# Kernel optimization log

Measured on AMD Instinct MI355X. Metric: run time of the kernel, lower is better.

Reference implementation:

```python
import jax, jax.numpy as jnp
import numpy as np

B, C, D_MODEL, N_HEADS = 2, 2048, 1024, 16


def rotary_matrix(context_length: int, d: int) -> jnp.ndarray:
    """Faithful vectorization of get_rotary_matrix: theta = 10000^(-2*(i-1)/d)."""
    half = d // 2
    i = jnp.arange(half, dtype=jnp.float32)
    theta = 10000.0 ** (-2.0 * (i - 1.0) / d)          # note the (i-1), as in source
    m = jnp.arange(context_length, dtype=jnp.float32)
    ang = m[:, None] * theta                            # [C, d/2]
    c, s = jnp.cos(ang), jnp.sin(ang)
    ev = 2 * jnp.arange(half)
    od = ev + 1
    R = jnp.zeros((context_length, d, d), jnp.float32)
    R = R.at[:, ev, ev].set(c)
    R = R.at[:, ev, od].set(-s)
    R = R.at[:, od, ev].set(s)
    R = R.at[:, od, od].set(c)
    return R


def setup_inputs() -> dict:
    key = jax.random.key(0)
    k1, k2, k3, k4 = jax.random.split(key, 4)
    x = jax.random.normal(k1, (B, C, D_MODEL), dtype=jnp.float32)
    w_qkv = jax.random.normal(k2, (3 * D_MODEL, D_MODEL), dtype=jnp.float32) * 0.02
    w_out = jax.random.normal(k3, (D_MODEL, D_MODEL), dtype=jnp.float32) * 0.02
    b_out = jax.random.normal(k4, (D_MODEL,), dtype=jnp.float32) * 0.02
    return {"x": x, "w_qkv": w_qkv, "w_out": w_out, "b_out": b_out}


def reference(x, w_qkv, w_out, b_out):
    b, c, d = x.shape
    h = N_HEADS
    dh = d // h
    qkv = x @ w_qkv.T                                   # [B,C,3D]
    q, k, v = jnp.split(qkv, 3, axis=-1)
    # [B,C,D] -> [B,H,C,dh]
    q = q.reshape(b, c, h, dh).transpose(0, 2, 1, 3)
    k = k.reshape(b, c, h, dh).transpose(0, 2, 1, 3)
    v = v.reshape(b, c, h, dh).transpose(0, 2, 1, 3)
    R = rotary_matrix(c, dh)                            # [C,dh,dh]
    q_rot = jnp.einsum('bhci,cij->bhcj', q, R)
    k_rot = jnp.einsum('bhci,cij->bhcj', k, R)
    scale = jnp.sqrt(jnp.float32(dh))
    # exact math of the source: exp with no max subtraction, separate num/den
    attn_num = jnp.exp(jnp.einsum('bhqd,bhkd->bhqk', q_rot, k_rot) / scale)
    attn_den = jnp.exp(jnp.einsum('bhqd,bhkd->bhqk', q, k) / scale)
    attn_den = jnp.sum(attn_den, axis=-1, keepdims=True)
    attn = attn_num / attn_den
    causal = jnp.tril(jnp.ones((c, c), jnp.float32))[None, None]
    attn = jnp.where(causal == 0, 0.0, attn)
    y = jnp.einsum('bhqk,bhkd->bhqd', attn, v)
    y = y.transpose(0, 2, 1, 3).reshape(b, c, d)
    return y @ w_out.T + b_out
```

## Files before the change

kernel.cpp:

```cpp
#include <hip/hip_runtime.h>
#include <math.h>
#include <stdint.h>

#define BB 2
#define CC 2048
#define DD 1024
#define HH 16
#define DHH 64
#define HALF 32

typedef __attribute__((ext_vector_type(8))) short bf16x8;
typedef __attribute__((ext_vector_type(4))) float f32x4;
typedef unsigned int u32;

__device__ __forceinline__ ushort f2bf(float f) {
    uint32_t u = __builtin_bit_cast(uint32_t, f);
    u = (u + 0x7FFFu + ((u >> 16) & 1u)) >> 16;
    return (ushort)u;
}
__device__ __forceinline__ float bf2f(ushort u) {
    return __builtin_bit_cast(float, ((uint32_t)u) << 16);
}

__device__ __forceinline__ void gload16(const void* g, void* lds) {
    __builtin_amdgcn_global_load_lds(
        (const u32 __attribute__((address_space(1)))*)g,
        (u32 __attribute__((address_space(3)))*)lds, 16, 0, 0);
}

__global__ __launch_bounds__(256) void cast_bf16_k(const float* __restrict__ src,
                                                   ushort* __restrict__ dst, int n8) {
    int id = blockIdx.x * 256 + threadIdx.x;
    if (id >= n8) return;
    float4 a = *reinterpret_cast<const float4*>(src + (size_t)id * 8);
    float4 b = *reinterpret_cast<const float4*>(src + (size_t)id * 8 + 4);
    bf16x8 o;
    o[0] = (short)f2bf(a.x); o[1] = (short)f2bf(a.y);
    o[2] = (short)f2bf(a.z); o[3] = (short)f2bf(a.w);
    o[4] = (short)f2bf(b.x); o[5] = (short)f2bf(b.y);
    o[6] = (short)f2bf(b.z); o[7] = (short)f2bf(b.w);
    *reinterpret_cast<bf16x8*>(dst + (size_t)id * 8) = o;
}

__global__ __launch_bounds__(256) void rope_table_k(float* __restrict__ ct, float* __restrict__ st) {
    int idx = blockIdx.x * 256 + threadIdx.x;
    if (idx >= CC * HALF) return;
    int m = idx >> 5;
    int t = idx & 31;
    double theta_d = pow(10000.0, -2.0 * ((double)t - 1.0) / 64.0);
    float theta = (float)theta_d;
    float ang = (float)m * theta;
    ct[idx] = cosf(ang);
    st[idx] = sinf(ang);
}

__global__ __launch_bounds__(256) void qkv_gemm_mfma_k(const ushort* __restrict__ xb,
                                                       const ushort* __restrict__ wqb,
                                                       ushort* __restrict__ q,
                                                       ushort* __restrict__ k,
                                                       ushort* __restrict__ vT) {
    __shared__ ushort Al[128 * 64];
    __shared__ ushort Bl[128 * 64];
    const int tid = threadIdx.x;
    const int w = tid >> 6, l = tid & 63;
    const int l15 = l & 15, lg = l >> 4;
    const int wr = w >> 1, wc = w & 1;
    const int m0 = blockIdx.x * 128, n0 = blockIdx.y * 128;
    const int lrow = l >> 3, lch = l & 7;

    f32x4 acc[4][4];
#pragma unroll
    for (int i = 0; i < 4; i++)
#pragma unroll
        for (int j = 0; j < 4; j++) acc[i][j] = (f32x4){0.f, 0.f, 0.f, 0.f};

    for (int k0 = 0; k0 < 1024; k0 += 64) {
        __syncthreads();
#pragma unroll
        for (int c = 0; c < 4; c++) {
            int row = w * 32 + c * 8 + lrow;
            int gch = (lch ^ (row & 7)) * 8;
            gload16(xb + (size_t)(m0 + row) * 1024 + k0 + gch, &Al[(w * 32 + c * 8) * 64]);
            gload16(wqb + (size_t)(n0 + row) * 1024 + k0 + gch, &Bl[(w * 32 + c * 8) * 64]);
        }
        __syncthreads();
#pragma unroll
        for (int kk = 0; kk < 2; kk++) {
            bf16x8 a[4], b[4];
#pragma unroll
            for (int mt = 0; mt < 4; mt++) {
                int row = wr * 64 + mt * 16 + l15;
                a[mt] = *reinterpret_cast<const bf16x8*>(&Al[row * 64 + ((kk * 4 + lg) ^ (row & 7)) * 8]);
            }
#pragma unroll
            for (int nt = 0; nt < 4; nt++) {
                int row = wc * 64 + nt * 16 + l15;
                b[nt] = *reinterpret_cast<const bf16x8*>(&Bl[row * 64 + ((kk * 4 + lg) ^ (row & 7)) * 8]);
            }
#pragma unroll
            for (int mt = 0; mt < 4; mt++)
#pragma unroll
                for (int nt = 0; nt < 4; nt++)
                    acc[mt][nt] = __builtin_amdgcn_mfma_f32_16x16x32_bf16(a[mt], b[nt], acc[mt][nt], 0, 0, 0);
        }
    }
#pragma unroll
    for (int mt = 0; mt < 4; mt++)
#pragma unroll
        for (int nt = 0; nt < 4; nt++) {
            int n = n0 + wc * 64 + nt * 16 + l15;
            int part = n >> 10;
            int d = n & 1023;
            int h = d >> 6, dd = d & 63;
            int mbase = m0 + wr * 64 + mt * 16 + lg * 4;
            int bb = mbase >> 11, cpos = mbase & 2047;
            if (part == 2) {
                ushort4 pk;
                pk.x = f2bf(acc[mt][nt][0]); pk.y = f2bf(acc[mt][nt][1]);
                pk.z = f2bf(acc[mt][nt][2]); pk.w = f2bf(acc[mt][nt][3]);
                *reinterpret_cast<ushort4*>(vT + (((size_t)bb * HH + h) * DHH + dd) * CC + cpos) = pk;
            } else {
                ushort* dst = (part == 0) ? q : k;
#pragma unroll
                for (int r = 0; r < 4; r++)
                    dst[(((size_t)bb * HH + h) * CC + (cpos + r)) * DHH + dd] = f2bf(acc[mt][nt][r]);
            }
        }
}

__global__ __launch_bounds__(256) void rot_k(const ushort* __restrict__ q, const ushort* __restrict__ k,
                                             const float* __restrict__ ct, const float* __restrict__ st,
                                             ushort* __restrict__ qr, ushort* __restrict__ kr) {
    int id = blockIdx.x * 256 + threadIdx.x;
    int oct = id & 7;
    int c = (id >> 3) & 2047;
    int bh = id >> 14;
    size_t base = ((size_t)bh * CC + c) * DHH + oct * 8;
    bf16x8 q8 = *reinterpret_cast<const bf16x8*>(q + base);
    bf16x8 k8 = *reinterpret_cast<const bf16x8*>(k + base);
    float4 c4 = *reinterpret_cast<const float4*>(ct + c * 32 + oct * 4);
    float4 s4 = *reinterpret_cast<const float4*>(st + c * 32 + oct * 4);
    float cc[4] = {c4.x, c4.y, c4.z, c4.w};
    float ss[4] = {s4.x, s4.y, s4.z, s4.w};
    bf16x8 qo, ko;
#pragma unroll
    for (int p = 0; p < 4; p++) {
        float qe = bf2f((ushort)q8[2 * p]), qd = bf2f((ushort)q8[2 * p + 1]);
        float ke = bf2f((ushort)k8[2 * p]), kd = bf2f((ushort)k8[2 * p + 1]);
        qo[2 * p]     = (short)f2bf(qe * cc[p] + qd * ss[p]);
        qo[2 * p + 1] = (short)f2bf(qd * cc[p] - qe * ss[p]);
        ko[2 * p]     = (short)f2bf(ke * cc[p] + kd * ss[p]);
        ko[2 * p + 1] = (short)f2bf(kd * cc[p] - ke * ss[p]);
    }
    *reinterpret_cast<bf16x8*>(qr + base) = qo;
    *reinterpret_cast<bf16x8*>(kr + base) = ko;
}

#define PSTR 76
__global__ __launch_bounds__(256) void attn_mfma_k(const ushort* __restrict__ qg,
                                                   const ushort* __restrict__ kg,
                                                   const ushort* __restrict__ vTg,
                                                   const ushort* __restrict__ qrg,
                                                   const ushort* __restrict__ krg,
                                                   ushort* __restrict__ y) {
    __shared__ ushort Kl[64 * 64];
    __shared__ ushort Krl[64 * 64];
    __shared__ ushort Vt[64 * 64];
    __shared__ ushort Pl[4][16 * PSTR];

    const int tid = threadIdx.x;
    const int w = tid >> 6, l = tid & 63;
    const int l15 = l & 15, lg = l >> 4;
    const int lrow = l >> 3, lch = l & 7;
    const int bid = blockIdx.x;
    const int bh = bid >> 5;
    const int xt = bid & 31;
    const int tile = (bid & 512) ? (31 - xt) : xt;
    const int q0 = tile * 64;
    const ushort* qb  = qg  + (size_t)bh * CC * DHH;
    const ushort* kb  = kg  + (size_t)bh * CC * DHH;
    const ushort* vTb = vTg + (size_t)bh * DHH * CC;
    const ushort* qrb = qrg + (size_t)bh * CC * DHH;
    const ushort* krb = krg + (size_t)bh * CC * DHH;

    bf16x8 qf[2], qrf[2];
#pragma unroll
    for (int kk = 0; kk < 2; kk++) {
        int row = q0 + w * 16 + l15;
        qf[kk]  = *reinterpret_cast<const bf16x8*>(qb  + (size_t)row * DHH + kk * 32 + lg * 8);
        qrf[kk] = *reinterpret_cast<const bf16x8*>(qrb + (size_t)row * DHH + kk * 32 + lg * 8);
    }

    f32x4 yacc[4];
    float dacc[4];
#pragma unroll
    for (int nt = 0; nt < 4; nt++) yacc[nt] = (f32x4){0.f, 0.f, 0.f, 0.f};
#pragma unroll
    for (int r = 0; r < 4; r++) dacc[r] = 0.f;

    for (int kt = 0; kt < CC / 64; kt++) {
        const int k0 = kt * 64;
        const bool need = (k0 <= q0 + 63);
        __syncthreads();
#pragma unroll
        for (int c = 0; c < 2; c++) {
            int row = w * 16 + c * 8 + lrow;
            int gch = (lch ^ (row & 7)) * 8;
            gload16(kb + (size_t)(k0 + row) * DHH + gch, &Kl[(w * 16 + c * 8) * 64]);
            if (need) {
                gload16(krb + (size_t)(k0 + row) * DHH + gch, &Krl[(w * 16 + c * 8) * 64]);
                gload16(vTb + (size_t)row * CC + k0 + gch, &Vt[(w * 16 + c * 8) * 64]);
            }
        }
        __syncthreads();

#pragma unroll
        for (int nt = 0; nt < 4; nt++) {
            f32x4 s = (f32x4){0.f, 0.f, 0.f, 0.f};
#pragma unroll
            for (int kk = 0; kk < 2; kk++) {
                int row = nt * 16 + l15;
                bf16x8 bk = *reinterpret_cast<const bf16x8*>(&Kl[row * 64 + ((kk * 4 + lg) ^ (row & 7)) * 8]);
                s = __builtin_amdgcn_mfma_f32_16x16x32_bf16(qf[kk], bk, s, 0, 0, 0);
            }
#pragma unroll
            for (int r = 0; r < 4; r++) dacc[r] += exp2f(s[r] * 0.1803368801f);
        }

        if (need) {
#pragma unroll
            for (int nt = 0; nt < 4; nt++) {
                f32x4 s = (f32x4){0.f, 0.f, 0.f, 0.f};
#pragma unroll
                for (int kk = 0; kk < 2; kk++) {
                    int row = nt * 16 + l15;
                    bf16x8 bk = *reinterpret_cast<const bf16x8*>(&Krl[row * 64 + ((kk * 4 + lg) ^ (row & 7)) * 8]);
                    s = __builtin_amdgcn_mfma_f32_16x16x32_bf16(qrf[kk], bk, s, 0, 0, 0);
                }
#pragma unroll
                for (int r = 0; r < 4; r++) {
                    int qrow = q0 + w * 16 + lg * 4 + r;
                    int key = k0 + nt * 16 + l15;
                    float p = (key <= qrow) ? exp2f(s[r] * 0.1803368801f) : 0.f;
                    Pl[w][(lg * 4 + r) * PSTR + nt * 16 + l15] = f2bf(p);
                }
            }
            bf16x8 pa[2];
#pragma unroll
            for (int kk2 = 0; kk2 < 2; kk2++)
                pa[kk2] = *reinterpret_cast<const bf16x8*>(&Pl[w][l15 * PSTR + kk2 * 32 + lg * 8]);
#pragma unroll
            for (int nt2 = 0; nt2 < 4; nt2++)
#pragma unroll
                for (int kk2 = 0; kk2 < 2; kk2++) {
                    int row = nt2 * 16 + l15;
                    bf16x8 bv = *reinterpret_cast<const bf16x8*>(&Vt[row * 64 + ((kk2 * 4 + lg) ^ (row & 7)) * 8]);
                    yacc[nt2] = __builtin_amdgcn_mfma_f32_16x16x32_bf16(pa[kk2], bv, yacc[nt2], 0, 0, 0);
                }
        }
    }

#pragma unroll
    for (int r = 0; r < 4; r++) {
        float vsum = dacc[r];
#pragma unroll
        for (int msk = 1; msk < 16; msk <<= 1) vsum += __shfl_xor(vsum, msk, 64);
        dacc[r] = vsum;
    }

    const int b = bh >> 4, h = bh & 15;
#pragma unroll
    for (int r = 0; r < 4; r++) {
        int row = q0 + w * 16 + lg * 4 + r;
        float inv = 1.f / dacc[r];
#pragma unroll
        for (int nt2 = 0; nt2 < 4; nt2++) {
            int d = nt2 * 16 + l15;
            y[((size_t)b * CC + row) * DD + h * DHH + d] = f2bf(yacc[nt2][r] * inv);
        }
    }
}

__global__ __launch_bounds__(256) void out_proj_mfma_k(const ushort* __restrict__ yb,
                                                       const ushort* __restrict__ wob,
                                                       const float* __restrict__ bias,
                                                       float* __restrict__ out) {
    __shared__ ushort Al[128 * 64];
    __shared__ ushort Bl[128 * 64];
    const int tid = threadIdx.x;
    const int w = tid >> 6, l = tid & 63;
    const int l15 = l & 15, lg = l >> 4;
    const int wr = w >> 1, wc = w & 1;
    const int m0 = blockIdx.x * 128, n0 = blockIdx.y * 128;
    const int lrow = l >> 3, lch = l & 7;

    f32x4 acc[4][4];
#pragma unroll
    for (int i = 0; i < 4; i++)
#pragma unroll
        for (int j = 0; j < 4; j++) acc[i][j] = (f32x4){0.f, 0.f, 0.f, 0.f};

    for (int k0 = 0; k0 < 1024; k0 += 64) {
        __syncthreads();
#pragma unroll
        for (int c = 0; c < 4; c++) {
            int row = w * 32 + c * 8 + lrow;
            int gch = (lch ^ (row & 7)) * 8;
            gload16(yb + (size_t)(m0 + row) * 1024 + k0 + gch, &Al[(w * 32 + c * 8) * 64]);
            gload16(wob + (size_t)(n0 + row) * 1024 + k0 + gch, &Bl[(w * 32 + c * 8) * 64]);
        }
        __syncthreads();
#pragma unroll
        for (int kk = 0; kk < 2; kk++) {
            bf16x8 a[4], b[4];
#pragma unroll
            for (int mt = 0; mt < 4; mt++) {
                int row = wr * 64 + mt * 16 + l15;
                a[mt] = *reinterpret_cast<const bf16x8*>(&Al[row * 64 + ((kk * 4 + lg) ^ (row & 7)) * 8]);
            }
#pragma unroll
            for (int nt = 0; nt < 4; nt++) {
                int row = wc * 64 + nt * 16 + l15;
                b[nt] = *reinterpret_cast<const bf16x8*>(&Bl[row * 64 + ((kk * 4 + lg) ^ (row & 7)) * 8]);
            }
#pragma unroll
            for (int mt = 0; mt < 4; mt++)
#pragma unroll
                for (int nt = 0; nt < 4; nt++)
                    acc[mt][nt] = __builtin_amdgcn_mfma_f32_16x16x32_bf16(a[mt], b[nt], acc[mt][nt], 0, 0, 0);
        }
    }
#pragma unroll
    for (int mt = 0; mt < 4; mt++)
#pragma unroll
        for (int nt = 0; nt < 4; nt++) {
            int n = n0 + wc * 64 + nt * 16 + l15;
            float bv = bias[n];
#pragma unroll
            for (int r = 0; r < 4; r++) {
                int m = m0 + wr * 64 + mt * 16 + lg * 4 + r;
                out[(size_t)m * 1024 + n] = acc[mt][nt][r] + bv;
            }
        }
}

extern "C" void kernel_launch(void* const* d_in, const int* in_sizes, int n_in,
                              void* d_out, int out_size, void* d_ws, size_t ws_size,
                              hipStream_t stream) {
    (void)in_sizes; (void)n_in; (void)out_size; (void)ws_size;
    const float* x     = (const float*)d_in[0];
    const float* w_qkv = (const float*)d_in[1];
    const float* w_out = (const float*)d_in[2];
    const float* b_out = (const float*)d_in[3];
    float* out = (float*)d_out;

    char* p = (char*)d_ws;
    float* ct = (float*)p;  p += (size_t)CC * HALF * 4;
    float* st = (float*)p;  p += (size_t)CC * HALF * 4;
    ushort* xb  = (ushort*)p; p += (size_t)4096 * 1024 * 2;
    ushort* wqb = (ushort*)p; p += (size_t)3072 * 1024 * 2;
    ushort* wob = (ushort*)p; p += (size_t)1024 * 1024 * 2;
    const size_t TEN = (size_t)BB * HH * CC * DHH;
    ushort* qb = (ushort*)p; p += TEN * 2;
    ushort* kb = (ushort*)p; p += TEN * 2;
    ushort* vT = (ushort*)p; p += TEN * 2;
    ushort* qr = (ushort*)p; p += TEN * 2;
    ushort* kr = (ushort*)p; p += TEN * 2;
    ushort* yb = (ushort*)p; p += (size_t)4096 * 1024 * 2;

    cast_bf16_k<<<dim3(2048), dim3(256), 0, stream>>>(x, xb, 524288);
    cast_bf16_k<<<dim3(1536), dim3(256), 0, stream>>>(w_qkv, wqb, 393216);
    cast_bf16_k<<<dim3(512),  dim3(256), 0, stream>>>(w_out, wob, 131072);
    rope_table_k<<<dim3((CC * HALF) / 256), dim3(256), 0, stream>>>(ct, st);
    qkv_gemm_mfma_k<<<dim3(32, 24), dim3(256), 0, stream>>>(xb, wqb, qb, kb, vT);
    rot_k<<<dim3(2048), dim3(256), 0, stream>>>(qb, kb, ct, st, qr, kr);
    attn_mfma_k<<<dim3(1024), dim3(256), 0, stream>>>(qb, kb, vT, qr, kr, yb);
    out_proj_mfma_k<<<dim3(32, 8), dim3(256), 0, stream>>>(yb, wob, b_out, out);
}
```

Before: 179.6 us.

## Fuse RoPE into QKV GEMM epilogue and double-buffer attention K/V tiles

The separate rotary kernel is removed. The rotation is now applied in the QKV GEMM epilogue, using a lane shuffle to fetch the even/odd partner, and q/k plus qr/kr are written directly. The attention kernel double-buffers its K, Kr and V LDS tiles so the next tile loads while the current one computes, and it swaps the MFMA operand order so the score tile is transposed. That transposition lets the denominator reduction drop to two shuffles and lets P be written as packed 8-byte stores. The cost is doubled LDS use, which may lower occupancy, plus extra scattered table reads in the GEMM epilogue.

```diff
diff --git a/kernel.cpp b/kernel.cpp
--- a/kernel.cpp
+++ b/kernel.cpp
@@ -56,8 +56,12 @@
 
 __global__ __launch_bounds__(256) void qkv_gemm_mfma_k(const ushort* __restrict__ xb,
                                                        const ushort* __restrict__ wqb,
+                                                       const float* __restrict__ ct,
+                                                       const float* __restrict__ st,
                                                        ushort* __restrict__ q,
                                                        ushort* __restrict__ k,
+                                                       ushort* __restrict__ qr,
+                                                       ushort* __restrict__ kr,
                                                        ushort* __restrict__ vT) {
     __shared__ ushort Al[128 * 64];
     __shared__ ushort Bl[128 * 64];
@@ -120,52 +124,35 @@
                 pk.z = f2bf(acc[mt][nt][2]); pk.w = f2bf(acc[mt][nt][3]);
                 *reinterpret_cast<ushort4*>(vT + (((size_t)bb * HH + h) * DHH + dd) * CC + cpos) = pk;
             } else {
-                ushort* dst = (part == 0) ? q : k;
-#pragma unroll
-                for (int r = 0; r < 4; r++)
-                    dst[(((size_t)bb * HH + h) * CC + (cpos + r)) * DHH + dd] = f2bf(acc[mt][nt][r]);
-            }
-        }
-}
-
-__global__ __launch_bounds__(256) void rot_k(const ushort* __restrict__ q, const ushort* __restrict__ k,
-                                             const float* __restrict__ ct, const float* __restrict__ st,
-                                             ushort* __restrict__ qr, ushort* __restrict__ kr) {
-    int id = blockIdx.x * 256 + threadIdx.x;
-    int oct = id & 7;
-    int c = (id >> 3) & 2047;
-    int bh = id >> 14;
-    size_t base = ((size_t)bh * CC + c) * DHH + oct * 8;
-    bf16x8 q8 = *reinterpret_cast<const bf16x8*>(q + base);
-    bf16x8 k8 = *reinterpret_cast<const bf16x8*>(k + base);
-    float4 c4 = *reinterpret_cast<const float4*>(ct + c * 32 + oct * 4);
-    float4 s4 = *reinterpret_cast<const float4*>(st + c * 32 + oct * 4);
-    float cc[4] = {c4.x, c4.y, c4.z, c4.w};
-    float ss[4] = {s4.x, s4.y, s4.z, s4.w};
-    bf16x8 qo, ko;
-#pragma unroll
-    for (int p = 0; p < 4; p++) {
-        float qe = bf2f((ushort)q8[2 * p]), qd = bf2f((ushort)q8[2 * p + 1]);
-        float ke = bf2f((ushort)k8[2 * p]), kd = bf2f((ushort)k8[2 * p + 1]);
-        qo[2 * p]     = (short)f2bf(qe * cc[p] + qd * ss[p]);
-        qo[2 * p + 1] = (short)f2bf(qd * cc[p] - qe * ss[p]);
-        ko[2 * p]     = (short)f2bf(ke * cc[p] + kd * ss[p]);
-        ko[2 * p + 1] = (short)f2bf(kd * cc[p] - ke * ss[p]);
-    }
-    *reinterpret_cast<bf16x8*>(qr + base) = qo;
-    *reinterpret_cast<bf16x8*>(kr + base) = ko;
-}
-
-#define PSTR 76
+                ushort* dstu = (part == 0) ? q : k;
+                ushort* dstr = (part == 0) ? qr : kr;
+                const float sgn = (dd & 1) ? -1.f : 1.f;
+                const int t = dd >> 1;
+#pragma unroll
+                for (int r = 0; r < 4; r++) {
+                    float val = acc[mt][nt][r];
+                    float par = __shfl_xor(val, 1, 64);
+                    float c = ct[(cpos + r) * 32 + t];
+                    float s = st[(cpos + r) * 32 + t];
+                    float rot = val * c + sgn * par * s;
+                    size_t base = (((size_t)bb * HH + h) * CC + (cpos + r)) * DHH + dd;
+                    dstu[base] = f2bf(val);
+                    dstr[base] = f2bf(rot);
+                }
+            }
+        }
+}
+
+#define PSTR 72
 __global__ __launch_bounds__(256) void attn_mfma_k(const ushort* __restrict__ qg,
                                                    const ushort* __restrict__ kg,
                                                    const ushort* __restrict__ vTg,
                                                    const ushort* __restrict__ qrg,
                                                    const ushort* __restrict__ krg,
                                                    ushort* __restrict__ y) {
-    __shared__ ushort Kl[64 * 64];
-    __shared__ ushort Krl[64 * 64];
-    __shared__ ushort Vt[64 * 64];
+    __shared__ ushort Kl[2][64 * 64];
+    __shared__ ushort Krl[2][64 * 64];
+    __shared__ ushort Vt[2][64 * 64];
     __shared__ ushort Pl[4][16 * PSTR];
 
     const int tid = threadIdx.x;
@@ -192,58 +179,70 @@
     }
 
     f32x4 yacc[4];
-    float dacc[4];
 #pragma unroll
     for (int nt = 0; nt < 4; nt++) yacc[nt] = (f32x4){0.f, 0.f, 0.f, 0.f};
-#pragma unroll
-    for (int r = 0; r < 4; r++) dacc[r] = 0.f;
+    float dacc = 0.f;
+
+#define STAGE(KT, BUF)                                                                     \
+    {                                                                                      \
+        const int sk0 = (KT) * 64;                                                         \
+        const bool sneed = (sk0 <= q0 + 63);                                               \
+        _Pragma("unroll")                                                                  \
+        for (int c = 0; c < 2; c++) {                                                      \
+            int row = w * 16 + c * 8 + lrow;                                               \
+            int gch = (lch ^ (row & 7)) * 8;                                               \
+            gload16(kb + (size_t)(sk0 + row) * DHH + gch, &Kl[BUF][(w * 16 + c * 8) * 64]);\
+            if (sneed) {                                                                   \
+                gload16(krb + (size_t)(sk0 + row) * DHH + gch, &Krl[BUF][(w * 16 + c * 8) * 64]); \
+                gload16(vTb + (size_t)row * CC + sk0 + gch, &Vt[BUF][(w * 16 + c * 8) * 64]);     \
+            }                                                                              \
+        }                                                                                  \
+    }
+
+    STAGE(0, 0);
+    __syncthreads();
+    int cur = 0;
 
     for (int kt = 0; kt < CC / 64; kt++) {
+        if (kt + 1 < CC / 64) STAGE(kt + 1, cur ^ 1);
         const int k0 = kt * 64;
         const bool need = (k0 <= q0 + 63);
-        __syncthreads();
-#pragma unroll
-        for (int c = 0; c < 2; c++) {
-            int row = w * 16 + c * 8 + lrow;
-            int gch = (lch ^ (row & 7)) * 8;
-            gload16(kb + (size_t)(k0 + row) * DHH + gch, &Kl[(w * 16 + c * 8) * 64]);
-            if (need) {
-                gload16(krb + (size_t)(k0 + row) * DHH + gch, &Krl[(w * 16 + c * 8) * 64]);
-                gload16(vTb + (size_t)row * CC + k0 + gch, &Vt[(w * 16 + c * 8) * 64]);
-            }
-        }
-        __syncthreads();
 
 #pragma unroll
         for (int nt = 0; nt < 4; nt++) {
             f32x4 s = (f32x4){0.f, 0.f, 0.f, 0.f};
 #pragma unroll
             for (int kk = 0; kk < 2; kk++) {
-                int row = nt * 16 + l15;
-                bf16x8 bk = *reinterpret_cast<const bf16x8*>(&Kl[row * 64 + ((kk * 4 + lg) ^ (row & 7)) * 8]);
-                s = __builtin_amdgcn_mfma_f32_16x16x32_bf16(qf[kk], bk, s, 0, 0, 0);
-            }
-#pragma unroll
-            for (int r = 0; r < 4; r++) dacc[r] += exp2f(s[r] * 0.1803368801f);
+                int krow = nt * 16 + l15;
+                bf16x8 ka = *reinterpret_cast<const bf16x8*>(&Kl[cur][krow * 64 + ((kk * 4 + lg) ^ (krow & 7)) * 8]);
+                s = __builtin_amdgcn_mfma_f32_16x16x32_bf16(ka, qf[kk], s, 0, 0, 0);
+            }
+#pragma unroll
+            for (int r = 0; r < 4; r++) dacc += exp2f(s[r] * 0.1803368801f);
         }
 
         if (need) {
+            const int qrow = q0 + w * 16 + l15;
 #pragma unroll
             for (int nt = 0; nt < 4; nt++) {
                 f32x4 s = (f32x4){0.f, 0.f, 0.f, 0.f};
 #pragma unroll
                 for (int kk = 0; kk < 2; kk++) {
-                    int row = nt * 16 + l15;
-                    bf16x8 bk = *reinterpret_cast<const bf16x8*>(&Krl[row * 64 + ((kk * 4 + lg) ^ (row & 7)) * 8]);
-                    s = __builtin_amdgcn_mfma_f32_16x16x32_bf16(qrf[kk], bk, s, 0, 0, 0);
+                    int krow = nt * 16 + l15;
+                    bf16x8 ka = *reinterpret_cast<const bf16x8*>(&Krl[cur][krow * 64 + ((kk * 4 + lg) ^ (krow & 7)) * 8]);
+                    s = __builtin_amdgcn_mfma_f32_16x16x32_bf16(ka, qrf[kk], s, 0, 0, 0);
                 }
+                ushort pb[4];
 #pragma unroll
                 for (int r = 0; r < 4; r++) {
-                    int qrow = q0 + w * 16 + lg * 4 + r;
-                    int key = k0 + nt * 16 + l15;
+                    int key = k0 + nt * 16 + lg * 4 + r;
                     float p = (key <= qrow) ? exp2f(s[r] * 0.1803368801f) : 0.f;
-                    Pl[w][(lg * 4 + r) * PSTR + nt * 16 + l15] = f2bf(p);
+                    pb[r] = f2bf(p);
                 }
+                uint2 pk;
+                pk.x = (u32)pb[0] | ((u32)pb[1] << 16);
+                pk.y = (u32)pb[2] | ((u32)pb[3] << 16);
+                *reinterpret_cast<uint2*>(&Pl[w][l15 * PSTR + nt * 16 + lg * 4]) = pk;
             }
             bf16x8 pa[2];
 #pragma unroll
@@ -253,32 +252,30 @@
             for (int nt2 = 0; nt2 < 4; nt2++)
 #pragma unroll
                 for (int kk2 = 0; kk2 < 2; kk2++) {
-                    int row = nt2 * 16 + l15;
-                    bf16x8 bv = *reinterpret_cast<const bf16x8*>(&Vt[row * 64 + ((kk2 * 4 + lg) ^ (row & 7)) * 8]);
+                    int vrow = nt2 * 16 + l15;
+                    bf16x8 bv = *reinterpret_cast<const bf16x8*>(&Vt[cur][vrow * 64 + ((kk2 * 4 + lg) ^ (vrow & 7)) * 8]);
                     yacc[nt2] = __builtin_amdgcn_mfma_f32_16x16x32_bf16(pa[kk2], bv, yacc[nt2], 0, 0, 0);
                 }
         }
-    }
-
+        __syncthreads();
+        cur ^= 1;
+    }
+
+    float den = dacc;
+    den += __shfl_xor(den, 16, 64);
+    den += __shfl_xor(den, 32, 64);
+
+    const int b = bh >> 4, h = bh & 15;
 #pragma unroll
     for (int r = 0; r < 4; r++) {
-        float vsum = dacc[r];
-#pragma unroll
-        for (int msk = 1; msk < 16; msk <<= 1) vsum += __shfl_xor(vsum, msk, 64);
-        dacc[r] = vsum;
-    }
-
-    const int b = bh >> 4, h = bh & 15;
-#pragma unroll
-    for (int r = 0; r < 4; r++) {
+        float dr = __shfl(den, lg * 4 + r, 64);
+        float inv = 1.f / dr;
         int row = q0 + w * 16 + lg * 4 + r;
-        float inv = 1.f / dacc[r];
-#pragma unroll
-        for (int nt2 = 0; nt2 < 4; nt2++) {
-            int d = nt2 * 16 + l15;
-            y[((size_t)b * CC + row) * DD + h * DHH + d] = f2bf(yacc[nt2][r] * inv);
-        }
-    }
+#pragma unroll
+        for (int nt2 = 0; nt2 < 4; nt2++)
+            y[((size_t)b * CC + row) * DD + h * DHH + nt2 * 16 + l15] = f2bf(yacc[nt2][r] * inv);
+    }
+#undef STAGE
 }
 
 __global__ __launch_bounds__(256) void out_proj_mfma_k(const ushort* __restrict__ yb,
@@ -372,8 +369,7 @@
     cast_bf16_k<<<dim3(1536), dim3(256), 0, stream>>>(w_qkv, wqb, 393216);
     cast_bf16_k<<<dim3(512),  dim3(256), 0, stream>>>(w_out, wob, 131072);
     rope_table_k<<<dim3((CC * HALF) / 256), dim3(256), 0, stream>>>(ct, st);
-    qkv_gemm_mfma_k<<<dim3(32, 24), dim3(256), 0, stream>>>(xb, wqb, qb, kb, vT);
-    rot_k<<<dim3(2048), dim3(256), 0, stream>>>(qb, kb, ct, st, qr, kr);
+    qkv_gemm_mfma_k<<<dim3(32, 24), dim3(256), 0, stream>>>(xb, wqb, ct, st, qb, kb, qr, kr, vT);
     attn_mfma_k<<<dim3(1024), dim3(256), 0, stream>>>(qb, kb, vT, qr, kr, yb);
     out_proj_mfma_k<<<dim3(32, 8), dim3(256), 0, stream>>>(yb, wob, b_out, out);
 }
```

Result: slower. 221.3 us (+23.2%).
